# Optimization experiments

Measured on AMD Instinct MI355X. Metric: run time of the kernel, lower is better.

The kernel has to match this reference:

```python
import math
import jax, jax.numpy as jnp
import numpy as np

NUM_HEAD = 16

def get_slopes(n):
    def pow2(n):
        start = 2 ** (-2 ** (-(math.log2(n) - 3)))
        return [start * start ** i for i in range(n)]
    if math.log2(n).is_integer():
        return pow2(n)
    c = 2 ** math.floor(math.log2(n))
    return pow2(c) + get_slopes(2 * c)[0::2][: n - c]

def setup_inputs() -> dict:
    key = jax.random.key(0)
    ks = jax.random.split(key, 9)
    B, T, C = 2, 2048, 2048
    x = jax.random.normal(ks[0], (B, T, C), dtype=jnp.float32)
    std = 0.02
    Wq = std * jax.random.normal(ks[1], (C, C), dtype=jnp.float32)
    Wk = std * jax.random.normal(ks[2], (C, C), dtype=jnp.float32)
    Wv = std * jax.random.normal(ks[3], (C, C), dtype=jnp.float32)
    Wo = (0.02 / np.sqrt(2 * 24)) * jax.random.normal(ks[4], (C, C), dtype=jnp.float32)
    bq = jnp.zeros((C,), jnp.float32)
    bk = jnp.zeros((C,), jnp.float32)
    bv = jnp.zeros((C,), jnp.float32)
    bo = jnp.zeros((C,), jnp.float32)
    return {"x": x, "Wq": Wq, "bq": bq, "Wk": Wk, "bk": bk,
            "Wv": Wv, "bv": bv, "Wo": Wo, "bo": bo}

def reference(x, Wq, bq, Wk, bk, Wv, bv, Wo, bo):
    B, T, C = x.shape
    H = NUM_HEAD
    D = C // H
    slopes = jnp.asarray(get_slopes(H), dtype=jnp.float32)  # [H]

    def split_heads(y):  # [B,T,C] -> [B,H,T,D]
        return y.reshape(B, T, H, D).transpose(0, 2, 1, 3)

    q = split_heads(x @ Wq + bq)
    k = split_heads(x @ Wk + bk)
    v = split_heads(x @ Wv + bv)

    attn = jnp.einsum("bhqd,bhkd->bhqk", q, k) / jnp.sqrt(jnp.float32(D))
    # ALiBi: bias[h, j] = slopes[h] * (j - (T-1)), broadcast over queries
    alibi = slopes[:, None, None] * (jnp.arange(T, dtype=jnp.float32) - (T - 1))[None, None, :]
    attn = attn + alibi  # [B,H,T,T] + [H,1,T]

    causal = jnp.tril(jnp.ones((T, T), dtype=bool))[None, None]
    attn = jnp.where(causal, attn, jnp.finfo(jnp.float32).min)
    p = jax.nn.softmax(attn, axis=-1)

    o = jnp.einsum("bhqk,bhkd->bhqd", p, v).transpose(0, 2, 1, 3).reshape(B, T, C)
    return o @ Wo + bo
```

## Files before the change

### kernel.cpp

```cpp
#include <hip/hip_runtime.h>
#include <math.h>


typedef unsigned short u16;
using bf16x8 = __attribute__((ext_vector_type(8))) short;
using f32x4  = __attribute__((ext_vector_type(4))) float;

__device__ __forceinline__ u16 f2bf(float f) {
  union { float f; unsigned u; } c; c.f = f;
  unsigned r = c.u + 0x7fffu + ((c.u >> 16) & 1u);
  return (u16)(r >> 16);
}
__device__ __forceinline__ float bf2f(u16 b) {
  union { unsigned u; float f; } c; c.u = ((unsigned)b) << 16; return c.f;
}
__device__ __forceinline__ unsigned cvtpk(float a, float b) {
  unsigned r;
  asm("v_cvt_pk_bf16_f32 %0, %1, %2" : "=v"(r) : "v"(a), "v"(b));
  return r;
}
__device__ __forceinline__ void g2l16(const void* g, void* l) {
  __builtin_amdgcn_global_load_lds(
      (const __attribute__((address_space(1))) void*)g,
      (__attribute__((address_space(3))) void*)l, 16, 0, 0);
}

__device__ __forceinline__ int band_jmin(int s, float slope2) {
  const int idist = (int)(36.0f / slope2);
  const int cut = 64 * s - idist - 31;
  return (cut > 0) ? (cut >> 5) : 0;
}

__global__ __launch_bounds__(256) void split_f32(const float* __restrict__ in,
                                                 u16* __restrict__ hi, int n4) {
  for (int i = blockIdx.x * 256 + threadIdx.x; i < n4; i += gridDim.x * 256) {
    const float4 v = ((const float4*)in)[i];
    ushort4 h;
    h.x = f2bf(v.x); h.y = f2bf(v.y); h.z = f2bf(v.z); h.w = f2bf(v.w);
    ((ushort4*)hi)[i] = h;
  }
}

__global__ __launch_bounds__(256) void tsplit4_f32(
    const float* __restrict__ W0, const float* __restrict__ W1,
    const float* __restrict__ W2, const float* __restrict__ W3,
    u16* __restrict__ D0, u16* __restrict__ D1,
    u16* __restrict__ D2, u16* __restrict__ D3,
    int N, int K, float sc0) {
  __shared__ float tile[64][68];
  const int z = blockIdx.z;
  const float* W = (z == 0) ? W0 : (z == 1) ? W1 : (z == 2) ? W2 : W3;
  u16* Wth = (z == 0) ? D0 : (z == 1) ? D1 : (z == 2) ? D2 : D3;
  const float sc = (z == 0) ? sc0 : 1.f;
  const int tid = threadIdx.x;
  const int k0 = blockIdx.y * 64, n0 = blockIdx.x * 64;
  const int rr = tid >> 4, cc = (tid & 15) * 4;
#pragma unroll
  for (int u = 0; u < 4; ++u) {
    const float4 v = *(const float4*)&W[(size_t)(k0 + rr + 16 * u) * N + n0 + cc];
    tile[rr + 16 * u][cc + 0] = v.x;
    tile[rr + 16 * u][cc + 1] = v.y;
    tile[rr + 16 * u][cc + 2] = v.z;
    tile[rr + 16 * u][cc + 3] = v.w;
  }
  __syncthreads();
#pragma unroll
  for (int u = 0; u < 4; ++u) {
    const int nn = rr + 16 * u;
    ushort4 h;
    h.x = f2bf(tile[cc + 0][nn] * sc);
    h.y = f2bf(tile[cc + 1][nn] * sc);
    h.z = f2bf(tile[cc + 2][nn] * sc);
    h.w = f2bf(tile[cc + 3][nn] * sc);
    *(ushort4*)&Wth[(size_t)(n0 + nn) * K + k0 + cc] = h;
  }
}

template <int MODE>
__global__ __launch_bounds__(512, 2) void gemm256(
    const u16* __restrict__ Ah, const u16* __restrict__ Bth,
    const float* __restrict__ bias, const float* __restrict__ bias2,
    float bsc, u16* __restrict__ outH, u16* __restrict__ outH2,
    float* __restrict__ outF, int MM, int NN, int KK) {
  __shared__ u16 LA[4][8192];
  __shared__ u16 LB[4][8192];

  const int tid = threadIdx.x;
  const int wave = tid >> 6, lane = tid & 63;
  const int g = lane >> 4, q15 = lane & 15;
  const int wr = wave >> 2, wc = wave & 3;
  const int m0 = blockIdx.y * 256, n0 = blockIdx.x * 256;
  const int NT = KK >> 5;
  const int sxg = ((g ^ ((q15 >> 1) & 3)) << 4);

  f32x4 acc[8][4];
#pragma unroll
  for (int f = 0; f < 8; ++f)
#pragma unroll
    for (int j = 0; j < 4; ++j) acc[f][j] = (f32x4){0.f, 0.f, 0.f, 0.f};

  auto stageA = [&](int t) {
    const int rb = t & 3;
#pragma unroll
    for (int l = 0; l < 2; ++l) {
      const int ch = l * 512 + tid;
      const int row = ch >> 2, slot = ch & 3;
      const size_t ga = (size_t)(m0 + row) * KK + t * 32 +
                        ((slot ^ ((row >> 1) & 3)) * 8);
      g2l16(Ah + ga, (char*)(LA[rb]) + ch * 16);
    }
  };
  auto stageB = [&](int t) {
    const int rb = t & 3;
#pragma unroll
    for (int l = 0; l < 2; ++l) {
      const int ch = l * 512 + tid;
      const int row = ch >> 2, slot = ch & 3;
      const size_t gb = (size_t)(n0 + row) * KK + t * 32 +
                        ((slot ^ ((row >> 1) & 3)) * 8);
      g2l16(Bth + gb, (char*)(LB[rb]) + ch * 16);
    }
  };

  stageA(0); stageB(0);
  __builtin_amdgcn_sched_barrier(0);
  if (NT > 1) { stageA(1); stageB(1); }
  __builtin_amdgcn_sched_barrier(0);
  if (NT > 2) { stageA(2); stageB(2); }
  __builtin_amdgcn_sched_barrier(0);
  if (NT > 2)      { asm volatile("s_waitcnt vmcnt(8)" ::: "memory"); }
  else if (NT > 1) { asm volatile("s_waitcnt vmcnt(4)" ::: "memory"); }
  else             { asm volatile("s_waitcnt vmcnt(0)" ::: "memory"); }
  __builtin_amdgcn_sched_barrier(0);
  __builtin_amdgcn_s_barrier();

  for (int t = 0; t < NT; ++t) {
    const int rb = t & 3;
    const char* baseA = (const char*)(LA[rb]);
    const char* baseB = (const char*)(LB[rb]);

    bf16x8 bf[4], af[4];
#pragma unroll
    for (int j = 0; j < 4; ++j)
      bf[j] = *(const bf16x8*)(baseB + (wc * 64 + j * 16 + q15) * 64 + sxg);
#pragma unroll
    for (int f = 0; f < 4; ++f)
      af[f] = *(const bf16x8*)(baseA + (wr * 128 + f * 16 + q15) * 64 + sxg);
    if (t + 3 < NT) stageA(t + 3);
    __builtin_amdgcn_sched_barrier(0);
    __builtin_amdgcn_s_barrier();
    asm volatile("s_waitcnt lgkmcnt(0)" ::: "memory");
    __builtin_amdgcn_sched_barrier(0);
    __builtin_amdgcn_s_setprio(1);
#pragma unroll
    for (int f = 0; f < 4; ++f)
#pragma unroll
      for (int j = 0; j < 4; ++j)
        acc[f][j] = __builtin_amdgcn_mfma_f32_16x16x32_bf16(
            af[f], bf[j], acc[f][j], 0, 0, 0);
    __builtin_amdgcn_s_setprio(0);
    __builtin_amdgcn_sched_barrier(0);
    __builtin_amdgcn_s_barrier();

    bf16x8 ag[4];
#pragma unroll
    for (int f = 0; f < 4; ++f)
      ag[f] = *(const bf16x8*)(baseA + (wr * 128 + 64 + f * 16 + q15) * 64 + sxg);
    if (t + 3 < NT) stageB(t + 3);
    __builtin_amdgcn_sched_barrier(0);
    __builtin_amdgcn_s_barrier();
    asm volatile("s_waitcnt lgkmcnt(0)" ::: "memory");
    __builtin_amdgcn_sched_barrier(0);
    __builtin_amdgcn_s_setprio(1);
#pragma unroll
    for (int f = 0; f < 4; ++f)
#pragma unroll
      for (int j = 0; j < 4; ++j)
        acc[4 + f][j] = __builtin_amdgcn_mfma_f32_16x16x32_bf16(
            ag[f], bf[j], acc[4 + f][j], 0, 0, 0);
    __builtin_amdgcn_s_setprio(0);
    if (t + 1 < NT) {
      if (t + 4 <= NT)      { asm volatile("s_waitcnt vmcnt(8)" ::: "memory"); }
      else if (t + 3 <= NT) { asm volatile("s_waitcnt vmcnt(4)" ::: "memory"); }
      else                  { asm volatile("s_waitcnt vmcnt(0)" ::: "memory"); }
    }
    __builtin_amdgcn_sched_barrier(0);
    __builtin_amdgcn_s_barrier();
  }

#pragma unroll
  for (int f = 0; f < 8; ++f)
#pragma unroll
    for (int j = 0; j < 4; ++j)
#pragma unroll
      for (int r = 0; r < 4; ++r) {
        const int row = m0 + wr * 128 + f * 16 + g * 4 + r;
        const int col = n0 + wc * 64 + j * 16 + q15;
        const float v = acc[f][j][r];
        if (MODE == 3) {
          const int sel = col >> 11;
          const int c2 = col & 2047;
          const float vv = v + (sel ? bias2[c2] : bias[c2] * bsc);
          const int bb = row >> 11, tt = row & 2047;
          const int hh = c2 >> 7, dd = c2 & 127;
          (sel ? outH2 : outH)[(((size_t)bb * 16 + hh) * 2048 + tt) * 128 + dd] =
              f2bf(vv);
        }
      }
}

template <int MODE>
__global__ __launch_bounds__(512) void gemm256x128(
    const u16* __restrict__ Ah, const u16* __restrict__ Bth,
    const float* __restrict__ bias, float bsc,
    u16* __restrict__ outH, float* __restrict__ outF,
    int MM, int NN, int KK) {
  __shared__ u16 LA[4][8192];
  __shared__ u16 LB[4][4096];

  const int tid = threadIdx.x;
  const int wave = tid >> 6, lane = tid & 63;
  const int g = lane >> 4, q15 = lane & 15;
  const int wr = wave >> 1, wc = wave & 1;
  const int m0 = blockIdx.y * 256, n0 = blockIdx.x * 128;
  const int NT = KK >> 5;
  const int sxg = ((g ^ ((q15 >> 1) & 3)) << 4);

  f32x4 acc[4][4];
#pragma unroll
  for (int f = 0; f < 4; ++f)
#pragma unroll
    for (int j = 0; j < 4; ++j) acc[f][j] = (f32x4){0.f, 0.f, 0.f, 0.f};

  auto stageA = [&](int t) {
    const int rb = t & 3;
#pragma unroll
    for (int l = 0; l < 2; ++l) {
      const int ch = l * 512 + tid;
      const int row = ch >> 2, slot = ch & 3;
      const size_t ga = (size_t)(m0 + row) * KK + t * 32 +
                        ((slot ^ ((row >> 1) & 3)) * 8);
      g2l16(Ah + ga, (char*)(LA[rb]) + ch * 16);
    }
  };
  auto stageB = [&](int t) {
    const int rb = t & 3;
    const int ch = tid;
    const int row = ch >> 2, slot = ch & 3;
    const size_t gb = (size_t)(n0 + row) * KK + t * 32 +
                      ((slot ^ ((row >> 1) & 3)) * 8);
    g2l16(Bth + gb, (char*)(LB[rb]) + ch * 16);
  };

  stageA(0); stageB(0);
  __builtin_amdgcn_sched_barrier(0);
  if (NT > 1) { stageA(1); stageB(1); }
  __builtin_amdgcn_sched_barrier(0);
  if (NT > 2) { stageA(2); stageB(2); }
  __builtin_amdgcn_sched_barrier(0);
  if (NT > 2)      { asm volatile("s_waitcnt vmcnt(6)" ::: "memory"); }
  else if (NT > 1) { asm volatile("s_waitcnt vmcnt(3)" ::: "memory"); }
  else             { asm volatile("s_waitcnt vmcnt(0)" ::: "memory"); }
  __builtin_amdgcn_sched_barrier(0);
  __builtin_amdgcn_s_barrier();

  for (int t = 0; t < NT; ++t) {
    const int rb = t & 3;
    const char* baseA = (const char*)(LA[rb]);
    const char* baseB = (const char*)(LB[rb]);

    bf16x8 af[4], bf[4];
#pragma unroll
    for (int f = 0; f < 4; ++f)
      af[f] = *(const bf16x8*)(baseA + (wr * 64 + f * 16 + q15) * 64 + sxg);
#pragma unroll
    for (int j = 0; j < 4; ++j)
      bf[j] = *(const bf16x8*)(baseB + (wc * 64 + j * 16 + q15) * 64 + sxg);
    if (t + 3 < NT) { stageA(t + 3); stageB(t + 3); }
    __builtin_amdgcn_sched_barrier(0);
    __builtin_amdgcn_s_barrier();
    asm volatile("s_waitcnt lgkmcnt(0)" ::: "memory");
    __builtin_amdgcn_sched_barrier(0);
    __builtin_amdgcn_s_setprio(1);
#pragma unroll
    for (int f = 0; f < 4; ++f)
#pragma unroll
      for (int j = 0; j < 4; ++j)
        acc[f][j] = __builtin_amdgcn_mfma_f32_16x16x32_bf16(
            af[f], bf[j], acc[f][j], 0, 0, 0);
    __builtin_amdgcn_s_setprio(0);
    if (t + 1 < NT) {
      if (t + 4 <= NT)      { asm volatile("s_waitcnt vmcnt(6)" ::: "memory"); }
      else if (t + 3 <= NT) { asm volatile("s_waitcnt vmcnt(3)" ::: "memory"); }
      else                  { asm volatile("s_waitcnt vmcnt(0)" ::: "memory"); }
    }
    __builtin_amdgcn_sched_barrier(0);
    __builtin_amdgcn_s_barrier();
  }

#pragma unroll
  for (int f = 0; f < 4; ++f)
#pragma unroll
    for (int j = 0; j < 4; ++j)
#pragma unroll
      for (int r = 0; r < 4; ++r) {
        const int row = m0 + wr * 64 + f * 16 + g * 4 + r;
        const int col = n0 + wc * 64 + j * 16 + q15;
        const float v = acc[f][j][r];
        if (MODE == 0) {
          outF[(size_t)row * NN + col] = v + bias[col] * bsc;
        } else {
          outH[(size_t)row * NN + col] = f2bf(v + bias[row] * bsc);
        }
      }
}

__global__ __launch_bounds__(128) void attn_splitk(
    const u16* __restrict__ Qh, const u16* __restrict__ Kh,
    const u16* __restrict__ Vth, u16* __restrict__ Oh,
    float* __restrict__ Obuf, float* __restrict__ mArr,
    float* __restrict__ lArr, int T, int NB, int BH) {
  __shared__ u16 KS[3][4096];

  const int tid = threadIdx.x;
  const int wid = tid >> 6, lane = tid & 63;
  const int g = lane >> 4, q15 = lane & 15;
  const int L = blockIdx.x;

  int bh, u;
  if (BH == 32) {
    const int k = L >> 8;
    const int c = L & 255;
    bh = (c + 5 * k) & 31;
    u = k * 8 + (c >> 5);
  } else {
    bh = L / 48;
    u = L % 48;
  }
  int s, half;
  if (u < 16)      { s = u;      half = 2; }
  else if (u < 32) { s = 47 - u; half = 0; }
  else             { s = 63 - u; half = 1; }

  const int b = bh >> 4, h = bh & 15;
  const float slope2 = exp2f(-0.5f * (float)(h + 1)) * 1.44269504f;
  const int jmin = band_jmin(s, slope2);
  const bool loEmpty = (jmin >= s + 1);

  if (half == 0 && loEmpty) return;

  int lo, hi;
  if (half == 2)      { lo = jmin;                hi = 2 * s + 2; }
  else if (half == 0) { lo = jmin;                hi = s + 1; }
  else                { lo = loEmpty ? jmin : (s + 1); hi = 2 * s + 2; }
  const int ns = hi - lo;
  const bool maskable = (half != 0);
  const bool normStore = (half == 2) || (half == 1 && loEmpty);

  const int qw0 = s * 64 + wid * 32;
  const size_t vrow0 = (size_t)h * 128;
  const size_t vcol0 = (size_t)b * T;
  const size_t kbase = (size_t)bh * T;

  bf16x8 qfr[2][4];
#pragma unroll
  for (int qf2 = 0; qf2 < 2; ++qf2) {
    const size_t rb = ((size_t)bh * T + qw0 + qf2 * 16 + q15) * 128;
#pragma unroll
    for (int ks = 0; ks < 4; ++ks)
      qfr[qf2][ks] = *(const bf16x8*)&Qh[rb + ks * 32 + g * 8];
  }

  f32x4 oacc[2][8];
#pragma unroll
  for (int a = 0; a < 2; ++a)
#pragma unroll
    for (int n = 0; n < 8; ++n) oacc[a][n] = (f32x4){0.f, 0.f, 0.f, 0.f};
  float m_st[2] = {-1e5f, -1e5f};
  float l_part[2] = {0.f, 0.f};

  float sc8[2][4];
#pragma unroll
  for (int jf = 0; jf < 2; ++jf)
#pragma unroll
    for (int r = 0; r < 4; ++r) sc8[jf][r] = slope2 * (float)(jf * 16 + r);

  auto stageK = [&](int jt, int bf) {
    const int j0 = jt * 32;
#pragma unroll
    for (int uu = 0; uu < 4; ++uu) {
      const int c = wid * 4 + uu;
      const int row = c * 4 + g;
      const int off = (q15 * 16) ^ ((row & 7) << 4);
      const size_t gb = (kbase + j0 + row) * 128;
      g2l16((const char*)(Kh + gb) + off, (char*)(KS[bf]) + c * 1024);
    }
  };
  auto loadV = [&](int jt, bf16x8 (&vf)[8]) {
    const int j0 = jt * 32;
#pragma unroll
    for (int nf = 0; nf < 8; ++nf)
      vf[nf] = *(const bf16x8*)
          &Vth[(vrow0 + nf * 16 + q15) * (size_t)NB + vcol0 + j0 + g * 8];
  };

  bf16x8 vfA[8], vfB[8];
  __builtin_amdgcn_sched_barrier(0);
  stageK(hi - 1, 0);
  if (ns > 1) stageK(hi - 2, 1);
  __builtin_amdgcn_sched_barrier(0);
  loadV(hi - 1, vfA);
  asm volatile("s_waitcnt vmcnt(8)" ::: "memory");
  __builtin_amdgcn_sched_barrier(0);

  int cur = 0;

  auto ITER = [&](int it, bf16x8 (&vc)[8], bf16x8 (&vn)[8]) {
    const int jt = hi - 1 - it;
    const int j0 = jt * 32;
    __builtin_amdgcn_s_barrier();
    __builtin_amdgcn_sched_barrier(0);

    const bool haveV1 = (it + 1 < ns);
    const bool haveK2 = (it + 2 < ns);
    if (haveV1) loadV(jt - 1, vn);
    if (haveK2) {
      int nb = cur + 2; if (nb >= 3) nb -= 3;
      stageK(jt - 2, nb);
    }
    __builtin_amdgcn_sched_barrier(0);

    f32x4 sacc[2][2];
#pragma unroll
    for (int jf = 0; jf < 2; ++jf)
#pragma unroll
      for (int qf2 = 0; qf2 < 2; ++qf2) sacc[jf][qf2] = (f32x4){0.f, 0.f, 0.f, 0.f};
#pragma unroll
    for (int ks = 0; ks < 4; ++ks) {
      bf16x8 ka[2];
#pragma unroll
      for (int jf = 0; jf < 2; ++jf) {
        const int row = jf * 16 + q15;
        const int off = (row * 256 + ks * 64 + g * 16) ^ ((row & 7) << 4);
        ka[jf] = *(const bf16x8*)((const char*)(KS[cur]) + off);
      }
#pragma unroll
      for (int jf = 0; jf < 2; ++jf)
#pragma unroll
        for (int qf2 = 0; qf2 < 2; ++qf2)
          sacc[jf][qf2] = __builtin_amdgcn_mfma_f32_16x16x32_bf16(
              ka[jf], qfr[qf2][ks], sacc[jf][qf2], 0, 0, 0);
    }

    float a8[2][4];
    const float jb = (float)(j0 + 4 * g - (T - 1));
#pragma unroll
    for (int jf = 0; jf < 2; ++jf)
#pragma unroll
      for (int r = 0; r < 4; ++r) a8[jf][r] = fmaf(slope2, jb, sc8[jf][r]);

    unsigned Fw[2][4];
#pragma unroll
    for (int qf2 = 0; qf2 < 2; ++qf2) {
      const int qg = qw0 + qf2 * 16 + q15;
      float sv[2][4];
      float mt = -1e30f;
#pragma unroll
      for (int jf = 0; jf < 2; ++jf)
#pragma unroll
        for (int r = 0; r < 4; ++r) {
          float x = sacc[jf][qf2][r] + a8[jf][r];
          if (maskable && it < 2) {
            const int jg = j0 + jf * 16 + 4 * g + r;
            x = (jg > qg) ? -1e30f : x;
          }
          sv[jf][r] = x;
          mt = fmaxf(mt, x);
        }
      if (!__all(mt <= m_st[qf2] + 11.0f)) {
        mt = fmaxf(mt, __shfl_xor(mt, 16));
        mt = fmaxf(mt, __shfl_xor(mt, 32));
        const float mnew = fmaxf(m_st[qf2], mt);
        const float scl = exp2f(m_st[qf2] - mnew);
        l_part[qf2] *= scl;
        m_st[qf2] = mnew;
#pragma unroll
        for (int r = 0; r < 4; ++r) {
          const float sc = __shfl(scl, g * 4 + r);
#pragma unroll
          for (int nf = 0; nf < 8; ++nf) oacc[qf2][nf][r] *= sc;
        }
      }
      float rs = 0.f;
      float p[2][4];
#pragma unroll
      for (int jf = 0; jf < 2; ++jf)
#pragma unroll
        for (int r = 0; r < 4; ++r) {
          p[jf][r] = exp2f(sv[jf][r] - m_st[qf2]);
          rs += p[jf][r];
        }
      l_part[qf2] += rs;
      const unsigned W00 = cvtpk(p[0][0], p[0][1]), W01 = cvtpk(p[0][2], p[0][3]);
      const unsigned W10 = cvtpk(p[1][0], p[1][1]), W11 = cvtpk(p[1][2], p[1][3]);
      const int srcA = q15 + ((g & 1) << 5);
      const int srcB = srcA + 16;
      const unsigned A0 = (unsigned)__shfl((int)W00, srcA);
      const unsigned A1 = (unsigned)__shfl((int)W01, srcA);
      const unsigned B0 = (unsigned)__shfl((int)W00, srcB);
      const unsigned B1 = (unsigned)__shfl((int)W01, srcB);
      const unsigned C0 = (unsigned)__shfl((int)W10, srcA);
      const unsigned C1 = (unsigned)__shfl((int)W11, srcA);
      const unsigned D0 = (unsigned)__shfl((int)W10, srcB);
      const unsigned D1 = (unsigned)__shfl((int)W11, srcB);
      const bool hi2 = g >= 2;
      Fw[qf2][0] = hi2 ? C0 : A0;
      Fw[qf2][1] = hi2 ? C1 : A1;
      Fw[qf2][2] = hi2 ? D0 : B0;
      Fw[qf2][3] = hi2 ? D1 : B1;
    }

    if (haveV1) {
      if (haveK2) { asm volatile("s_waitcnt vmcnt(12)" ::: "memory"); }
      else        { asm volatile("s_waitcnt vmcnt(8)"  ::: "memory"); }
    } else        { asm volatile("s_waitcnt vmcnt(0)"  ::: "memory"); }
    __builtin_amdgcn_sched_barrier(0);

    union { unsigned uu[4]; bf16x8 v; } pa0, pa1;
#pragma unroll
    for (int w = 0; w < 4; ++w) { pa0.uu[w] = Fw[0][w]; pa1.uu[w] = Fw[1][w]; }
#pragma unroll
    for (int nf = 0; nf < 8; ++nf) {
      oacc[0][nf] = __builtin_amdgcn_mfma_f32_16x16x32_bf16(pa0.v, vc[nf], oacc[0][nf], 0, 0, 0);
      oacc[1][nf] = __builtin_amdgcn_mfma_f32_16x16x32_bf16(pa1.v, vc[nf], oacc[1][nf], 0, 0, 0);
    }

    cur = (cur == 2) ? 0 : cur + 1;
  };

  for (int it = 0; it < ns;) {
    ITER(it, vfA, vfB); ++it;
    if (it >= ns) break;
    ITER(it, vfB, vfA); ++it;
  }

  float lrow[2];
#pragma unroll
  for (int qf2 = 0; qf2 < 2; ++qf2) {
    float lr = l_part[qf2];
    lr += __shfl_xor(lr, 16);
    lr += __shfl_xor(lr, 32);
    lrow[qf2] = lr;
  }

  if (normStore) {
#pragma unroll
    for (int qf2 = 0; qf2 < 2; ++qf2) {
      const float inv = 1.0f / lrow[qf2];
#pragma unroll
      for (int r = 0; r < 4; ++r) {
        const float iv = __shfl(inv, g * 4 + r);
        const int qrow = qw0 + qf2 * 16 + g * 4 + r;
        const size_t ob = ((size_t)b * T + qrow) * 2048 + h * 128;
#pragma unroll
        for (int nf = 0; nf < 8; ++nf)
          Oh[ob + nf * 16 + q15] = f2bf(oacc[qf2][nf][r] * iv);
      }
    }
  } else {
    const int sp = s - 16;
    const size_t sbase = ((size_t)(bh * 16 + sp) * 2 + half) * 64;
    if (g == 0) {
#pragma unroll
      for (int qf2 = 0; qf2 < 2; ++qf2) {
        mArr[sbase + wid * 32 + qf2 * 16 + q15] = m_st[qf2];
        lArr[sbase + wid * 32 + qf2 * 16 + q15] = lrow[qf2];
      }
    }
    const size_t obase = sbase * 128;
#pragma unroll
    for (int qf2 = 0; qf2 < 2; ++qf2)
#pragma unroll
      for (int r = 0; r < 4; ++r) {
        const int row = wid * 32 + qf2 * 16 + g * 4 + r;
#pragma unroll
        for (int nf = 0; nf < 8; ++nf)
          Obuf[obase + (size_t)row * 128 + nf * 16 + q15] = oacc[qf2][nf][r];
      }
  }
}

__global__ __launch_bounds__(128) void combine_halves(
    const float* __restrict__ Obuf, const float* __restrict__ mArr,
    const float* __restrict__ lArr, u16* __restrict__ Oh, int T) {
  const int idx = blockIdx.x;
  const int row = idx & 63;
  const int sp = (idx >> 6) & 15;
  const int bh = idx >> 10;
  const int d = threadIdx.x;
  const int s = sp + 16;
  const int b = bh >> 4, h = bh & 15;
  const float slope2 = exp2f(-0.5f * (float)(h + 1)) * 1.44269504f;
  if (band_jmin(s, slope2) >= s + 1) return;
  const size_t sbase = ((size_t)(bh * 16 + sp) * 2) * 64;
  const float m1 = mArr[sbase + row],      l1 = lArr[sbase + row];
  const float m2 = mArr[sbase + 64 + row], l2 = lArr[sbase + 64 + row];
  const float M = fmaxf(m1, m2);
  const float w1 = exp2f(m1 - M), w2 = exp2f(m2 - M);
  const float inv = 1.0f / (l1 * w1 + l2 * w2);
  const size_t ob = sbase * 128;
  const float o1 = Obuf[ob + (size_t)row * 128 + d];
  const float o2 = Obuf[ob + 8192 + (size_t)row * 128 + d];
  const float v = (o1 * w1 + o2 * w2) * inv;
  const int qrow = s * 64 + row;
  Oh[((size_t)b * T + qrow) * 2048 + h * 128 + d] = f2bf(v);
}

#define TM 128
#define BKG 8

template <int QKV>
__global__ __launch_bounds__(256) void gemm_f32(
    const float* __restrict__ A, const float* __restrict__ W,
    const float* __restrict__ bias, float* __restrict__ out,
    int M, int N, int K, int T) {
  __shared__ float As[BKG][TM];
  __shared__ float Bs[BKG][TM];
  const int tid = threadIdx.x;
  const int tx = tid & 15, ty = tid >> 4;
  const int m0 = blockIdx.y * TM, n0 = blockIdx.x * TM;
  float acc[8][8];
#pragma unroll
  for (int i = 0; i < 8; ++i)
#pragma unroll
    for (int j = 0; j < 8; ++j) acc[i][j] = 0.f;
  const int arow = tid >> 1, acol = (tid & 1) * 4;
  const int brow = tid >> 5, bcol = (tid & 31) * 4;
  for (int k0 = 0; k0 < K; k0 += BKG) {
    const float4 av = *(const float4*)&A[(size_t)(m0 + arow) * K + k0 + acol];
    const float4 bv = *(const float4*)&W[(size_t)(k0 + brow) * N + n0 + bcol];
    __syncthreads();
    As[acol + 0][arow] = av.x; As[acol + 1][arow] = av.y;
    As[acol + 2][arow] = av.z; As[acol + 3][arow] = av.w;
    *(float4*)&Bs[brow][bcol] = bv;
    __syncthreads();
#pragma unroll
    for (int kk = 0; kk < BKG; ++kk) {
      const float4 a0 = *(const float4*)&As[kk][ty * 4];
      const float4 a1 = *(const float4*)&As[kk][64 + ty * 4];
      const float4 b0 = *(const float4*)&Bs[kk][tx * 4];
      const float4 b1 = *(const float4*)&Bs[kk][64 + tx * 4];
      const float af[8] = {a0.x, a0.y, a0.z, a0.w, a1.x, a1.y, a1.z, a1.w};
      const float bf[8] = {b0.x, b0.y, b0.z, b0.w, b1.x, b1.y, b1.z, b1.w};
#pragma unroll
      for (int i = 0; i < 8; ++i)
#pragma unroll
        for (int j = 0; j < 8; ++j) acc[i][j] += af[i] * bf[j];
    }
  }
#pragma unroll
  for (int a = 0; a < 2; ++a)
#pragma unroll
    for (int i = 0; i < 4; ++i) {
      const int row = m0 + a * 64 + ty * 4 + i;
      const int bb = row / T, t = row % T;
#pragma unroll
      for (int bj = 0; bj < 2; ++bj) {
        const int col = n0 + bj * 64 + tx * 4;
        float4 r;
        r.x = acc[a * 4 + i][bj * 4 + 0] + bias[col + 0];
        r.y = acc[a * 4 + i][bj * 4 + 1] + bias[col + 1];
        r.z = acc[a * 4 + i][bj * 4 + 2] + bias[col + 2];
        r.w = acc[a * 4 + i][bj * 4 + 3] + bias[col + 3];
        if (QKV) {
          const int hh = col >> 7, dd = col & 127;
          *(float4*)&out[(((size_t)bb * 16 + hh) * T + t) * 128 + dd] = r;
        } else {
          *(float4*)&out[(size_t)row * N + col] = r;
        }
      }
    }
}

#define QT 32
#define KT 32
#define DP 132

__global__ __launch_bounds__(256) void flash_f32(
    const float* __restrict__ Q, const float* __restrict__ K,
    const float* __restrict__ V, float* __restrict__ O, int T) {
  __shared__ float Qs[QT][DP];
  __shared__ float Ks[KT][DP];
  __shared__ float Vs[KT][DP];
  __shared__ float Ps[QT][KT + 1];
  const int tid = threadIdx.x;
  const int jh = tid & 15, ih = tid >> 4;
  const int bh = blockIdx.y;
  const int h = bh & 15;
  const int q0 = blockIdx.x * QT;
  const float slope = exp2f(-0.5f * (float)(h + 1));
  const float rsD = 0.08838834764831845f;
  {
    const float* Qg = Q + ((size_t)bh * T + q0) * 128;
    const int r = tid >> 3, p = tid & 7;
#pragma unroll
    for (int u = 0; u < 4; ++u)
      *(float4*)&Qs[r][(p + 8 * u) * 4] = *(const float4*)&Qg[r * 128 + (p + 8 * u) * 4];
  }
  float m_st[2] = {-1e30f, -1e30f};
  float l_st[2] = {0.f, 0.f};
  float accv[2][8] = {};
  const int ktiles = blockIdx.x + 1;
  for (int kt = 0; kt < ktiles; ++kt) {
    const int j0 = kt * KT;
    const float* Kg = K + ((size_t)bh * T + j0) * 128;
    const float* Vg = V + ((size_t)bh * T + j0) * 128;
    __syncthreads();
    {
      const int r = tid >> 3, p = tid & 7;
#pragma unroll
      for (int u = 0; u < 4; ++u) {
        *(float4*)&Ks[r][(p + 8 * u) * 4] = *(const float4*)&Kg[r * 128 + (p + 8 * u) * 4];
        *(float4*)&Vs[r][(p + 8 * u) * 4] = *(const float4*)&Vg[r * 128 + (p + 8 * u) * 4];
      }
    }
    __syncthreads();
    float s00 = 0.f, s01 = 0.f, s10 = 0.f, s11 = 0.f;
#pragma unroll 8
    for (int d4 = 0; d4 < 32; ++d4) {
      const float4 qa = *(const float4*)&Qs[2 * ih + 0][4 * d4];
      const float4 qb = *(const float4*)&Qs[2 * ih + 1][4 * d4];
      const float4 ka = *(const float4*)&Ks[2 * jh + 0][4 * d4];
      const float4 kb = *(const float4*)&Ks[2 * jh + 1][4 * d4];
      s00 += qa.x * ka.x + qa.y * ka.y + qa.z * ka.z + qa.w * ka.w;
      s01 += qa.x * kb.x + qa.y * kb.y + qa.z * kb.z + qa.w * kb.w;
      s10 += qb.x * ka.x + qb.y * ka.y + qb.z * ka.z + qb.w * ka.w;
      s11 += qb.x * kb.x + qb.y * kb.y + qb.z * kb.z + qb.w * kb.w;
    }
    float sc[2][2] = {{s00, s01}, {s10, s11}};
    float mt[2];
#pragma unroll
    for (int r = 0; r < 2; ++r) {
      const int qg = q0 + 2 * ih + r;
#pragma unroll
      for (int c = 0; c < 2; ++c) {
        const int jg = j0 + 2 * jh + c;
        const float svv = sc[r][c] * rsD + slope * (float)(jg - (T - 1));
        sc[r][c] = (jg > qg) ? -1e30f : svv;
      }
      mt[r] = fmaxf(sc[r][0], sc[r][1]);
    }
#pragma unroll
    for (int m = 1; m < 16; m <<= 1) {
      mt[0] = fmaxf(mt[0], __shfl_xor(mt[0], m));
      mt[1] = fmaxf(mt[1], __shfl_xor(mt[1], m));
    }
#pragma unroll
    for (int r = 0; r < 2; ++r) {
      const float mnew = fmaxf(m_st[r], mt[r]);
      const float scl = (m_st[r] > -1e29f) ? expf(m_st[r] - mnew) : 0.f;
      const float p0 = expf(sc[r][0] - mnew);
      const float p1 = expf(sc[r][1] - mnew);
      float rs = p0 + p1;
#pragma unroll
      for (int m = 1; m < 16; m <<= 1) rs += __shfl_xor(rs, m);
      l_st[r] = l_st[r] * scl + rs;
      m_st[r] = mnew;
#pragma unroll
      for (int d = 0; d < 8; ++d) accv[r][d] *= scl;
      Ps[2 * ih + r][2 * jh + 0] = p0;
      Ps[2 * ih + r][2 * jh + 1] = p1;
    }
    __syncthreads();
#pragma unroll 4
    for (int j = 0; j < KT; ++j) {
      const float p0 = Ps[2 * ih + 0][j];
      const float p1 = Ps[2 * ih + 1][j];
      const float4 v0 = *(const float4*)&Vs[j][8 * jh];
      const float4 v1 = *(const float4*)&Vs[j][8 * jh + 4];
      accv[0][0] += p0 * v0.x; accv[0][1] += p0 * v0.y;
      accv[0][2] += p0 * v0.z; accv[0][3] += p0 * v0.w;
      accv[0][4] += p0 * v1.x; accv[0][5] += p0 * v1.y;
      accv[0][6] += p0 * v1.z; accv[0][7] += p0 * v1.w;
      accv[1][0] += p1 * v0.x; accv[1][1] += p1 * v0.y;
      accv[1][2] += p1 * v0.z; accv[1][3] += p1 * v0.w;
      accv[1][4] += p1 * v1.x; accv[1][5] += p1 * v1.y;
      accv[1][6] += p1 * v1.z; accv[1][7] += p1 * v1.w;
    }
  }
  const int b = bh >> 4;
#pragma unroll
  for (int r = 0; r < 2; ++r) {
    const int qg = q0 + 2 * ih + r;
    const float inv = 1.0f / l_st[r];
    float4 o0, o1;
    o0.x = accv[r][0] * inv; o0.y = accv[r][1] * inv;
    o0.z = accv[r][2] * inv; o0.w = accv[r][3] * inv;
    o1.x = accv[r][4] * inv; o1.y = accv[r][5] * inv;
    o1.z = accv[r][6] * inv; o1.w = accv[r][7] * inv;
    float* dst = O + ((size_t)b * T + qg) * 2048 + h * 128 + 8 * jh;
    *(float4*)&dst[0] = o0;
    *(float4*)&dst[4] = o1;
  }
}

extern "C" void kernel_launch(void* const* d_in, const int* in_sizes, int n_in,
                              void* d_out, int out_size, void* d_ws,
                              size_t ws_size, hipStream_t stream) {
  const float* x  = (const float*)d_in[0];
  const float* Wq = (const float*)d_in[1];
  const float* bq = (const float*)d_in[2];
  const float* Wk = (const float*)d_in[3];
  const float* bk = (const float*)d_in[4];
  const float* Wv = (const float*)d_in[5];
  const float* bv = (const float*)d_in[6];
  const float* Wo = (const float*)d_in[7];
  const float* bo = (const float*)d_in[8];
  float* out = (float*)d_out;

  const int C = 2048, T = 2048, H = 16;
  const int M = in_sizes[0] / C;
  const int B = M / T;
  const int BH = B * H;
  const size_t MC = (size_t)M * C, CC = (size_t)C * C;
  const size_t splitO = (size_t)BH * 16 * 2 * 8192;
  const size_t splitML = (size_t)BH * 16 * 2 * 64;
  const size_t need = (5 * MC + 4 * CC) * sizeof(u16) +
                      (splitO + 2 * splitML) * sizeof(float);

  const float QSC = 0.08838834764831845f * 1.44269504088896f;

  if (ws_size >= need && (M % 256) == 0) {
    u16* p = (u16*)d_ws;
    u16* xh   = p; p += MC;
    u16* wqth = p; p += CC;
    u16* wkth = p; p += CC;
    u16* wvth = p; p += CC;
    u16* woth = p; p += CC;
    u16* qh   = p; p += MC;
    u16* kh   = p; p += MC;
    u16* vth  = p; p += MC;
    u16* oh   = p; p += MC;
    float* Obuf = (float*)p;
    float* mArr = Obuf + splitO;
    float* lArr = mArr + splitML;

    split_f32<<<1024, 256, 0, stream>>>(x, xh, (int)(MC / 4));
    dim3 tg(C / 64, C / 64, 4);
    tsplit4_f32<<<tg, 256, 0, stream>>>(Wq, Wk, Wv, Wo, wqth, wkth, wvth,
                                        woth, C, C, QSC);

    dim3 gqk(2 * C / 256, M / 256);
    gemm256<3><<<gqk, 512, 0, stream>>>(xh, wqth, bq, bk, QSC, qh, kh,
                                        nullptr, M, 2 * C, C);
    dim3 gv(M / 128, C / 256);
    gemm256x128<2><<<gv, 512, 0, stream>>>(wvth, xh, bv, 1.f, vth, nullptr,
                                           C, M, C);

    attn_splitk<<<48 * BH, 128, 0, stream>>>(qh, kh, vth, oh, Obuf, mArr,
                                             lArr, T, M, BH);
    combine_halves<<<BH * 16 * 64, 128, 0, stream>>>(Obuf, mArr, lArr, oh, T);

    dim3 gq(C / 128, M / 256);
    gemm256x128<0><<<gq, 512, 0, stream>>>(oh, woth, bo, 1.f, nullptr, out,
                                           M, C, C);
  } else {
    float* Qw = (float*)d_ws;
    float* Kw = Qw + MC;
    float* Vw = Kw + MC;
    float* Ow = Vw + MC;
    dim3 ggrid(C / TM, M / TM);
    gemm_f32<1><<<ggrid, 256, 0, stream>>>(x, Wq, bq, Qw, M, C, C, T);
    gemm_f32<1><<<ggrid, 256, 0, stream>>>(x, Wk, bk, Kw, M, C, C, T);
    gemm_f32<1><<<ggrid, 256, 0, stream>>>(x, Wv, bv, Vw, M, C, C, T);
    dim3 fgrid(T / QT, B * H);
    flash_f32<<<fgrid, 256, 0, stream>>>(Qw, Kw, Vw, Ow, T);
    gemm_f32<0><<<ggrid, 256, 0, stream>>>(Ow, Wo, bo, out, M, C, C, T);
  }
}
```

Measured before the change: 298.6 us.

## Unify GEMMs into 256x128 triple-buffered kernel and raise occupancy

Replaces the 256x256 QK projection GEMM with a single 256x128 kernel template used for all projections. That kernel now uses three LDS buffers instead of four, prefetches two stages ahead instead of three, and requests four blocks per CU. The attention kernel gets a launch bound of 3 blocks per CU, and the ALiBi bias precompute arrays are folded into an fma on the score so fewer registers stay live. The aim is higher occupancy and less LDS per block, at the cost of less reuse per tile and a shallower prefetch that can expose memory latency.

```diff
diff --git a/kernel.cpp b/kernel.cpp
--- a/kernel.cpp
+++ b/kernel.cpp
@@ -77,76 +77,68 @@
 }
 
 template <int MODE>
-__global__ __launch_bounds__(512, 2) void gemm256(
+__global__ __launch_bounds__(512, 4) void gemm256x128(
     const u16* __restrict__ Ah, const u16* __restrict__ Bth,
     const float* __restrict__ bias, const float* __restrict__ bias2,
     float bsc, u16* __restrict__ outH, u16* __restrict__ outH2,
     float* __restrict__ outF, int MM, int NN, int KK) {
-  __shared__ u16 LA[4][8192];
-  __shared__ u16 LB[4][8192];
+  __shared__ u16 LA[3][8192];
+  __shared__ u16 LB[3][4096];
 
   const int tid = threadIdx.x;
   const int wave = tid >> 6, lane = tid & 63;
   const int g = lane >> 4, q15 = lane & 15;
-  const int wr = wave >> 2, wc = wave & 3;
-  const int m0 = blockIdx.y * 256, n0 = blockIdx.x * 256;
+  const int wr = wave >> 1, wc = wave & 1;
+  const int m0 = blockIdx.y * 256, n0 = blockIdx.x * 128;
   const int NT = KK >> 5;
   const int sxg = ((g ^ ((q15 >> 1) & 3)) << 4);
 
-  f32x4 acc[8][4];
-#pragma unroll
-  for (int f = 0; f < 8; ++f)
+  f32x4 acc[4][4];
+#pragma unroll
+  for (int f = 0; f < 4; ++f)
 #pragma unroll
     for (int j = 0; j < 4; ++j) acc[f][j] = (f32x4){0.f, 0.f, 0.f, 0.f};
 
-  auto stageA = [&](int t) {
-    const int rb = t & 3;
+  auto stageA = [&](int t, int rbuf) {
 #pragma unroll
     for (int l = 0; l < 2; ++l) {
       const int ch = l * 512 + tid;
       const int row = ch >> 2, slot = ch & 3;
       const size_t ga = (size_t)(m0 + row) * KK + t * 32 +
                         ((slot ^ ((row >> 1) & 3)) * 8);
-      g2l16(Ah + ga, (char*)(LA[rb]) + ch * 16);
+      g2l16(Ah + ga, (char*)(LA[rbuf]) + ch * 16);
     }
   };
-  auto stageB = [&](int t) {
-    const int rb = t & 3;
-#pragma unroll
-    for (int l = 0; l < 2; ++l) {
-      const int ch = l * 512 + tid;
-      const int row = ch >> 2, slot = ch & 3;
-      const size_t gb = (size_t)(n0 + row) * KK + t * 32 +
-                        ((slot ^ ((row >> 1) & 3)) * 8);
-      g2l16(Bth + gb, (char*)(LB[rb]) + ch * 16);
-    }
+  auto stageB = [&](int t, int rbuf) {
+    const int ch = tid;
+    const int row = ch >> 2, slot = ch & 3;
+    const size_t gb = (size_t)(n0 + row) * KK + t * 32 +
+                      ((slot ^ ((row >> 1) & 3)) * 8);
+    g2l16(Bth + gb, (char*)(LB[rbuf]) + ch * 16);
   };
 
-  stageA(0); stageB(0);
+  stageA(0, 0); stageB(0, 0);
   __builtin_amdgcn_sched_barrier(0);
-  if (NT > 1) { stageA(1); stageB(1); }
+  if (NT > 1) { stageA(1, 1); stageB(1, 1); }
   __builtin_amdgcn_sched_barrier(0);
-  if (NT > 2) { stageA(2); stageB(2); }
-  __builtin_amdgcn_sched_barrier(0);
-  if (NT > 2)      { asm volatile("s_waitcnt vmcnt(8)" ::: "memory"); }
-  else if (NT > 1) { asm volatile("s_waitcnt vmcnt(4)" ::: "memory"); }
-  else             { asm volatile("s_waitcnt vmcnt(0)" ::: "memory"); }
+  if (NT > 1) { asm volatile("s_waitcnt vmcnt(3)" ::: "memory"); }
+  else        { asm volatile("s_waitcnt vmcnt(0)" ::: "memory"); }
   __builtin_amdgcn_sched_barrier(0);
   __builtin_amdgcn_s_barrier();
 
+  int rb = 0, rb2 = 2;
   for (int t = 0; t < NT; ++t) {
-    const int rb = t & 3;
     const char* baseA = (const char*)(LA[rb]);
     const char* baseB = (const char*)(LB[rb]);
 
-    bf16x8 bf[4], af[4];
+    bf16x8 af[4], bf[4];
+#pragma unroll
+    for (int f = 0; f < 4; ++f)
+      af[f] = *(const bf16x8*)(baseA + (wr * 64 + f * 16 + q15) * 64 + sxg);
 #pragma unroll
     for (int j = 0; j < 4; ++j)
       bf[j] = *(const bf16x8*)(baseB + (wc * 64 + j * 16 + q15) * 64 + sxg);
-#pragma unroll
-    for (int f = 0; f < 4; ++f)
-      af[f] = *(const bf16x8*)(baseA + (wr * 128 + f * 16 + q15) * 64 + sxg);
-    if (t + 3 < NT) stageA(t + 3);
+    if (t + 2 < NT) { stageA(t + 2, rb2); stageB(t + 2, rb2); }
     __builtin_amdgcn_sched_barrier(0);
     __builtin_amdgcn_s_barrier();
     asm volatile("s_waitcnt lgkmcnt(0)" ::: "memory");
@@ -159,45 +151,30 @@
         acc[f][j] = __builtin_amdgcn_mfma_f32_16x16x32_bf16(
             af[f], bf[j], acc[f][j], 0, 0, 0);
     __builtin_amdgcn_s_setprio(0);
+    if (t + 1 < NT) {
+      if (t + 2 < NT) { asm volatile("s_waitcnt vmcnt(3)" ::: "memory"); }
+      else            { asm volatile("s_waitcnt vmcnt(0)" ::: "memory"); }
+    }
     __builtin_amdgcn_sched_barrier(0);
     __builtin_amdgcn_s_barrier();
-
-    bf16x8 ag[4];
-#pragma unroll
-    for (int f = 0; f < 4; ++f)
-      ag[f] = *(const bf16x8*)(baseA + (wr * 128 + 64 + f * 16 + q15) * 64 + sxg);
-    if (t + 3 < NT) stageB(t + 3);
-    __builtin_amdgcn_sched_barrier(0);
-    __builtin_amdgcn_s_barrier();
-    asm volatile("s_waitcnt lgkmcnt(0)" ::: "memory");
-    __builtin_amdgcn_sched_barrier(0);
-    __builtin_amdgcn_s_setprio(1);
-#pragma unroll
-    for (int f = 0; f < 4; ++f)
-#pragma unroll
-      for (int j = 0; j < 4; ++j)
-        acc[4 + f][j] = __builtin_amdgcn_mfma_f32_16x16x32_bf16(
-            ag[f], bf[j], acc[4 + f][j], 0, 0, 0);
-    __builtin_amdgcn_s_setprio(0);
-    if (t + 1 < NT) {
-      if (t + 4 <= NT)      { asm volatile("s_waitcnt vmcnt(8)" ::: "memory"); }
-      else if (t + 3 <= NT) { asm volatile("s_waitcnt vmcnt(4)" ::: "memory"); }
-      else                  { asm volatile("s_waitcnt vmcnt(0)" ::: "memory"); }
-    }
-    __builtin_amdgcn_sched_barrier(0);
-    __builtin_amdgcn_s_barrier();
-  }
-
-#pragma unroll
-  for (int f = 0; f < 8; ++f)
+    rb  = (rb  == 2) ? 0 : rb  + 1;
+    rb2 = (rb2 == 2) ? 0 : rb2 + 1;
+  }
+
+#pragma unroll
+  for (int f = 0; f < 4; ++f)
 #pragma unroll
     for (int j = 0; j < 4; ++j)
 #pragma unroll
       for (int r = 0; r < 4; ++r) {
-        const int row = m0 + wr * 128 + f * 16 + g * 4 + r;
+        const int row = m0 + wr * 64 + f * 16 + g * 4 + r;
         const int col = n0 + wc * 64 + j * 16 + q15;
         const float v = acc[f][j][r];
-        if (MODE == 3) {
+        if (MODE == 0) {
+          outF[(size_t)row * NN + col] = v + bias[col] * bsc;
+        } else if (MODE == 2) {
+          outH[(size_t)row * NN + col] = f2bf(v + bias[row] * bsc);
+        } else {
           const int sel = col >> 11;
           const int c2 = col & 2047;
           const float vv = v + (sel ? bias2[c2] : bias[c2] * bsc);
@@ -209,113 +186,7 @@
       }
 }
 
-template <int MODE>
-__global__ __launch_bounds__(512) void gemm256x128(
-    const u16* __restrict__ Ah, const u16* __restrict__ Bth,
-    const float* __restrict__ bias, float bsc,
-    u16* __restrict__ outH, float* __restrict__ outF,
-    int MM, int NN, int KK) {
-  __shared__ u16 LA[4][8192];
-  __shared__ u16 LB[4][4096];
-
-  const int tid = threadIdx.x;
-  const int wave = tid >> 6, lane = tid & 63;
-  const int g = lane >> 4, q15 = lane & 15;
-  const int wr = wave >> 1, wc = wave & 1;
-  const int m0 = blockIdx.y * 256, n0 = blockIdx.x * 128;
-  const int NT = KK >> 5;
-  const int sxg = ((g ^ ((q15 >> 1) & 3)) << 4);
-
-  f32x4 acc[4][4];
-#pragma unroll
-  for (int f = 0; f < 4; ++f)
-#pragma unroll
-    for (int j = 0; j < 4; ++j) acc[f][j] = (f32x4){0.f, 0.f, 0.f, 0.f};
-
-  auto stageA = [&](int t) {
-    const int rb = t & 3;
-#pragma unroll
-    for (int l = 0; l < 2; ++l) {
-      const int ch = l * 512 + tid;
-      const int row = ch >> 2, slot = ch & 3;
-      const size_t ga = (size_t)(m0 + row) * KK + t * 32 +
-                        ((slot ^ ((row >> 1) & 3)) * 8);
-      g2l16(Ah + ga, (char*)(LA[rb]) + ch * 16);
-    }
-  };
-  auto stageB = [&](int t) {
-    const int rb = t & 3;
-    const int ch = tid;
-    const int row = ch >> 2, slot = ch & 3;
-    const size_t gb = (size_t)(n0 + row) * KK + t * 32 +
-                      ((slot ^ ((row >> 1) & 3)) * 8);
-    g2l16(Bth + gb, (char*)(LB[rb]) + ch * 16);
-  };
-
-  stageA(0); stageB(0);
-  __builtin_amdgcn_sched_barrier(0);
-  if (NT > 1) { stageA(1); stageB(1); }
-  __builtin_amdgcn_sched_barrier(0);
-  if (NT > 2) { stageA(2); stageB(2); }
-  __builtin_amdgcn_sched_barrier(0);
-  if (NT > 2)      { asm volatile("s_waitcnt vmcnt(6)" ::: "memory"); }
-  else if (NT > 1) { asm volatile("s_waitcnt vmcnt(3)" ::: "memory"); }
-  else             { asm volatile("s_waitcnt vmcnt(0)" ::: "memory"); }
-  __builtin_amdgcn_sched_barrier(0);
-  __builtin_amdgcn_s_barrier();
-
-  for (int t = 0; t < NT; ++t) {
-    const int rb = t & 3;
-    const char* baseA = (const char*)(LA[rb]);
-    const char* baseB = (const char*)(LB[rb]);
-
-    bf16x8 af[4], bf[4];
-#pragma unroll
-    for (int f = 0; f < 4; ++f)
-      af[f] = *(const bf16x8*)(baseA + (wr * 64 + f * 16 + q15) * 64 + sxg);
-#pragma unroll
-    for (int j = 0; j < 4; ++j)
-      bf[j] = *(const bf16x8*)(baseB + (wc * 64 + j * 16 + q15) * 64 + sxg);
-    if (t + 3 < NT) { stageA(t + 3); stageB(t + 3); }
-    __builtin_amdgcn_sched_barrier(0);
-    __builtin_amdgcn_s_barrier();
-    asm volatile("s_waitcnt lgkmcnt(0)" ::: "memory");
-    __builtin_amdgcn_sched_barrier(0);
-    __builtin_amdgcn_s_setprio(1);
-#pragma unroll
-    for (int f = 0; f < 4; ++f)
-#pragma unroll
-      for (int j = 0; j < 4; ++j)
-        acc[f][j] = __builtin_amdgcn_mfma_f32_16x16x32_bf16(
-            af[f], bf[j], acc[f][j], 0, 0, 0);
-    __builtin_amdgcn_s_setprio(0);
-    if (t + 1 < NT) {
-      if (t + 4 <= NT)      { asm volatile("s_waitcnt vmcnt(6)" ::: "memory"); }
-      else if (t + 3 <= NT) { asm volatile("s_waitcnt vmcnt(3)" ::: "memory"); }
-      else                  { asm volatile("s_waitcnt vmcnt(0)" ::: "memory"); }
-    }
-    __builtin_amdgcn_sched_barrier(0);
-    __builtin_amdgcn_s_barrier();
-  }
-
-#pragma unroll
-  for (int f = 0; f < 4; ++f)
-#pragma unroll
-    for (int j = 0; j < 4; ++j)
-#pragma unroll
-      for (int r = 0; r < 4; ++r) {
-        const int row = m0 + wr * 64 + f * 16 + g * 4 + r;
-        const int col = n0 + wc * 64 + j * 16 + q15;
-        const float v = acc[f][j][r];
-        if (MODE == 0) {
-          outF[(size_t)row * NN + col] = v + bias[col] * bsc;
-        } else {
-          outH[(size_t)row * NN + col] = f2bf(v + bias[row] * bsc);
-        }
-      }
-}
-
-__global__ __launch_bounds__(128) void attn_splitk(
+__global__ __launch_bounds__(128, 3) void attn_splitk(
     const u16* __restrict__ Qh, const u16* __restrict__ Kh,
     const u16* __restrict__ Vth, u16* __restrict__ Oh,
     float* __restrict__ Obuf, float* __restrict__ mArr,
@@ -379,12 +250,6 @@
   float m_st[2] = {-1e5f, -1e5f};
   float l_part[2] = {0.f, 0.f};
 
-  float sc8[2][4];
-#pragma unroll
-  for (int jf = 0; jf < 2; ++jf)
-#pragma unroll
-    for (int r = 0; r < 4; ++r) sc8[jf][r] = slope2 * (float)(jf * 16 + r);
-
   auto stageK = [&](int jt, int bf) {
     const int j0 = jt * 32;
 #pragma unroll
@@ -452,12 +317,7 @@
               ka[jf], qfr[qf2][ks], sacc[jf][qf2], 0, 0, 0);
     }
 
-    float a8[2][4];
-    const float jb = (float)(j0 + 4 * g - (T - 1));
-#pragma unroll
-    for (int jf = 0; jf < 2; ++jf)
-#pragma unroll
-      for (int r = 0; r < 4; ++r) a8[jf][r] = fmaf(slope2, jb, sc8[jf][r]);
+    const float jb2 = (float)(j0 + 4 * g - (T - 1));
 
     unsigned Fw[2][4];
 #pragma unroll
@@ -469,7 +329,7 @@
       for (int jf = 0; jf < 2; ++jf)
 #pragma unroll
         for (int r = 0; r < 4; ++r) {
-          float x = sacc[jf][qf2][r] + a8[jf][r];
+          float x = fmaf(slope2, jb2 + (float)(jf * 16 + r), sacc[jf][qf2][r]);
           if (maskable && it < 2) {
             const int jg = j0 + jf * 16 + 4 * g + r;
             x = (jg > qg) ? -1e30f : x;
@@ -850,20 +710,20 @@
     tsplit4_f32<<<tg, 256, 0, stream>>>(Wq, Wk, Wv, Wo, wqth, wkth, wvth,
                                         woth, C, C, QSC);
 
-    dim3 gqk(2 * C / 256, M / 256);
-    gemm256<3><<<gqk, 512, 0, stream>>>(xh, wqth, bq, bk, QSC, qh, kh,
-                                        nullptr, M, 2 * C, C);
+    dim3 gqk(2 * C / 128, M / 256);
+    gemm256x128<3><<<gqk, 512, 0, stream>>>(xh, wqth, bq, bk, QSC, qh, kh,
+                                            nullptr, M, 2 * C, C);
     dim3 gv(M / 128, C / 256);
-    gemm256x128<2><<<gv, 512, 0, stream>>>(wvth, xh, bv, 1.f, vth, nullptr,
-                                           C, M, C);
+    gemm256x128<2><<<gv, 512, 0, stream>>>(wvth, xh, bv, nullptr, 1.f, vth,
+                                           nullptr, nullptr, C, M, C);
 
     attn_splitk<<<48 * BH, 128, 0, stream>>>(qh, kh, vth, oh, Obuf, mArr,
                                              lArr, T, M, BH);
     combine_halves<<<BH * 16 * 64, 128, 0, stream>>>(Obuf, mArr, lArr, oh, T);
 
     dim3 gq(C / 128, M / 256);
-    gemm256x128<0><<<gq, 512, 0, stream>>>(oh, woth, bo, 1.f, nullptr, out,
-                                           M, C, C);
+    gemm256x128<0><<<gq, 512, 0, stream>>>(oh, woth, bo, nullptr, 1.f,
+                                           nullptr, nullptr, out, M, C, C);
   } else {
     float* Qw = (float*)d_ws;
     float* Kw = Qw + MC;
```

Result: slower. 483.8 us (+62.0%).
